# Optimization experiments

Measured on AMD Instinct MI355X. Metric: run time of the kernel, lower is better.

The kernel has to match this reference:

```python
import jax, jax.numpy as jnp
import numpy as np

B, R, C, IC, OC = 32, 16384, 16, 16, 16  # batch, num_routes, num_capsules, in_ch, out_ch
NUM_ITERATIONS = 3


def squash(s, axis=-1):
    # scale * s / norm with scale = norm^2/(1+norm^2)  ==  norm/(1+norm^2) * s
    norm = jnp.linalg.norm(s, axis=axis, keepdims=True)
    return (norm / (1.0 + norm * norm)) * s


def setup_inputs() -> dict:
    key = jax.random.key(0)
    kx, kw = jax.random.split(key)
    x = jax.random.normal(kx, (B, C, IC), dtype=jnp.float32)
    # W param: torch shape (1, R, C, OC, IC); leading 1 squeezed here
    W = jax.random.normal(kw, (R, C, OC, IC), dtype=jnp.float32)
    return {"x": x, "W": W}


def reference(x, W):
    # u_hat[b,r,c,o] = sum_i W[r,c,o,i] * x[b,c,i]   (torch broadcast of x over routes)
    u_hat = jnp.einsum('rcoi,bci->brco', W, x)  # (B, R, C, OC)
    b = jnp.zeros((x.shape[0], R, C, 1), dtype=u_hat.dtype)
    outputs = None
    for it in range(NUM_ITERATIONS):
        c = jax.nn.softmax(b, axis=1)                      # softmax over routes
        s = (c * u_hat).sum(axis=1, keepdims=True)         # (B, 1, C, OC)
        outputs = squash(s)
        if it < NUM_ITERATIONS - 1:
            b = b + (u_hat * outputs).sum(axis=-1, keepdims=True)
    return outputs.squeeze(axis=1)  # (B, C, OC)
```

## Files before the change

### kernel.cpp

```cpp
#include <hip/hip_runtime.h>
#include <math.h>


typedef __attribute__((ext_vector_type(8)))  short short8;
typedef __attribute__((ext_vector_type(16))) float f32x16;

union FU { short8 s; unsigned int u[4]; };

__device__ __forceinline__ void splitpk(float a, float b,
                                        unsigned int& hp, unsigned int& lp) {
    unsigned int ua = __float_as_uint(a), ub = __float_as_uint(b);
    unsigned int ta = ua + 0x7FFFu + ((ua >> 16) & 1u);
    unsigned int tb = ub + 0x7FFFu + ((ub >> 16) & 1u);
    hp = (ta >> 16) | (tb & 0xFFFF0000u);
    float ha = __uint_as_float(ta & 0xFFFF0000u);
    float hb = __uint_as_float(tb & 0xFFFF0000u);
    unsigned int la = __float_as_uint(a - ha) + 0x8000u;
    unsigned int lb = __float_as_uint(b - hb) + 0x8000u;
    lp = (la >> 16) | (lb & 0xFFFF0000u);
}

__global__ __launch_bounds__(256) void k_zero(float* __restrict__ ws) {
    ws[blockIdx.x * 256 + threadIdx.x] = 0.f;
}

__global__ __launch_bounds__(256) void k_wsum(const float4* __restrict__ W4,
                                              float* __restrict__ wsum) {
    int gid = blockIdx.x * 256 + threadIdx.x;
    float4 acc = {0.f, 0.f, 0.f, 0.f};
    int idx = gid;
    #pragma unroll
    for (int it = 0; it < 64; ++it) {
        float4 w = W4[idx];
        acc.x += w.x; acc.y += w.y; acc.z += w.z; acc.w += w.w;
        idx += 262144;
    }
    int cls = gid & 1023;
    atomicAdd(&wsum[cls * 4 + 0], acc.x);
    atomicAdd(&wsum[cls * 4 + 1], acc.y);
    atomicAdd(&wsum[cls * 4 + 2], acc.z);
    atomicAdd(&wsum[cls * 4 + 3], acc.w);
}

__global__ __launch_bounds__(256) void k_v1(const float* __restrict__ wsum,
                                            const float* __restrict__ x,
                                            float* __restrict__ v1) {
    int t = blockIdx.x * 256 + threadIdx.x;
    int o = t & 15, c = (t >> 4) & 15, b = t >> 8;
    const float* xb = x + (b * 16 + c) * 16;
    const float* wr = wsum + (c * 16 + o) * 16;
    float s = 0.f;
    #pragma unroll
    for (int i = 0; i < 16; ++i) s += wr[i] * xb[i];
    s *= (1.0f / 16384.0f);
    float ns = s * s;
    #pragma unroll
    for (int d = 1; d < 16; d <<= 1) ns += __shfl_xor(ns, d);
    v1[t] = s * (sqrtf(ns) / (1.0f + ns));
}

__global__ __launch_bounds__(256) void k_vout_vs(const float* __restrict__ E,
                                                 const float* __restrict__ Z,
                                                 const float* __restrict__ v1,
                                                 float* __restrict__ vs) {
    int t = blockIdx.x * 256 + threadIdx.x;
    float s = E[t] / Z[t >> 4];
    float ns = s * s;
    #pragma unroll
    for (int d = 1; d < 16; d <<= 1) ns += __shfl_xor(ns, d);
    vs[t] = v1[t] + s * (sqrtf(ns) / (1.0f + ns));
}

__global__ __launch_bounds__(256) void k_vout(const float* __restrict__ E,
                                              const float* __restrict__ Z,
                                              float* __restrict__ dst) {
    int t = blockIdx.x * 256 + threadIdx.x;
    float s = E[t] / Z[t >> 4];
    float ns = s * s;
    #pragma unroll
    for (int d = 1; d < 16; d <<= 1) ns += __shfl_xor(ns, d);
    dst[t] = s * (sqrtf(ns) / (1.0f + ns));
}

__global__ __launch_bounds__(512)
void k_iter(const float* __restrict__ W,
            const float* __restrict__ x,
            const float* __restrict__ v,
            float* __restrict__ E,
            float* __restrict__ Z) {
    __shared__ float sV[512];
    __shared__ float E_lds[512];
    __shared__ float Z_lds[32];

    int c = blockIdx.y;
    int r0 = blockIdx.x * 256;
    int tid = threadIdx.x, wv = tid >> 6, l = tid & 63;
    int m  = l & 31;
    int hi = l >> 5;

    { int b = tid >> 4, o = tid & 15;
      sV[tid] = v[b * 256 + c * 16 + o];
      E_lds[tid] = 0.f; }
    if (tid < 32) Z_lds[tid] = 0.f;

    FU bh, bl;
    {
        const float4* xb = (const float4*)x + m * 64 + c * 4 + hi * 2;
        float4 x0 = xb[0], x1 = xb[1];
        splitpk(x0.x, x0.y, bh.u[0], bl.u[0]);
        splitpk(x0.z, x0.w, bh.u[1], bl.u[1]);
        splitpk(x1.x, x1.y, bh.u[2], bl.u[2]);
        splitpk(x1.z, x1.w, bh.u[3], bl.u[3]);
    }
    __syncthreads();

    float vf[16];
    #pragma unroll
    for (int reg = 0; reg < 16; ++reg) {
        int o = (reg & 3) + 4 * hi + 8 * ((reg >> 2) & 1);
        vf[reg] = sV[m * 16 + o];
    }

    float accE[16];
    #pragma unroll
    for (int reg = 0; reg < 16; ++reg) accE[reg] = 0.f;
    float accZ = 0.f;

    const float4* Wb = (const float4*)W +
        ((size_t)(r0 + wv * 2 + (m >> 4)) * 1024 + c * 64 + (m & 15) * 4 + hi * 2);

    float4 ca = Wb[0], cb = Wb[1];

    #pragma unroll
    for (int chunk = 0; chunk < 16; ++chunk) {
        float4 na = ca, nb = cb;
        if (chunk < 15) {
            na = Wb[(size_t)(chunk + 1) * 16384];
            nb = Wb[(size_t)(chunk + 1) * 16384 + 1];
        }

        FU ah, al;
        splitpk(ca.x, ca.y, ah.u[0], al.u[0]);
        splitpk(ca.z, ca.w, ah.u[1], al.u[1]);
        splitpk(cb.x, cb.y, ah.u[2], al.u[2]);
        splitpk(cb.z, cb.w, ah.u[3], al.u[3]);

        f32x16 cf;
        #pragma unroll
        for (int i = 0; i < 16; ++i) cf[i] = 0.f;
        cf = __builtin_amdgcn_mfma_f32_32x32x16_bf16(al.s, bl.s, cf, 0, 0, 0);
        cf = __builtin_amdgcn_mfma_f32_32x32x16_bf16(ah.s, bl.s, cf, 0, 0, 0);
        cf = __builtin_amdgcn_mfma_f32_32x32x16_bf16(al.s, bh.s, cf, 0, 0, 0);
        cf = __builtin_amdgcn_mfma_f32_32x32x16_bf16(ah.s, bh.s, cf, 0, 0, 0);

        float Lp0 = 0.f, Lp1 = 0.f;
        #pragma unroll
        for (int reg = 0; reg < 8; ++reg)  Lp0 += cf[reg] * vf[reg];
        #pragma unroll
        for (int reg = 8; reg < 16; ++reg) Lp1 += cf[reg] * vf[reg];
        float Lv0 = Lp0 + __shfl_xor(Lp0, 32);
        float Lv1 = Lp1 + __shfl_xor(Lp1, 32);
        float e0 = __expf(Lv0), e1 = __expf(Lv1);
        accZ += e0 + e1;
        #pragma unroll
        for (int reg = 0; reg < 8; ++reg)  accE[reg] += e0 * cf[reg];
        #pragma unroll
        for (int reg = 8; reg < 16; ++reg) accE[reg] += e1 * cf[reg];

        ca = na; cb = nb;
    }

    #pragma unroll
    for (int j = 0; j < 8; ++j) {
        int o = (j & 3) + 4 * hi + 8 * (j >> 2);
        atomicAdd(&E_lds[m * 16 + o], accE[j] + accE[j + 8]);
    }
    if (l < 32) atomicAdd(&Z_lds[m], accZ);
    __syncthreads();

    atomicAdd(&E[(tid >> 4) * 256 + c * 16 + (tid & 15)], E_lds[tid]);
    if (tid < 32) atomicAdd(&Z[tid * 16 + c], Z_lds[tid]);
}

extern "C" void kernel_launch(void* const* d_in, const int* in_sizes, int n_in,
                              void* d_out, int out_size, void* d_ws, size_t ws_size,
                              hipStream_t stream) {
    const float* x = (const float*)d_in[0];
    const float* W = (const float*)d_in[1];
    float* out = (float*)d_out;
    float* ws = (float*)d_ws;

    float* wsum = ws + 0;
    float* E2   = ws + 4096;
    float* Z2   = ws + 12288;
    float* E3   = ws + 12800;
    float* Z3   = ws + 20992;
    float* v1   = ws + 21504;
    float* vs   = ws + 29696;

    k_zero<<<84, 256, 0, stream>>>(ws);

    k_wsum<<<1024, 256, 0, stream>>>((const float4*)W, wsum);
    k_v1<<<32, 256, 0, stream>>>(wsum, x, v1);

    k_iter<<<dim3(64, 16), 512, 0, stream>>>(W, x, v1, E2, Z2);
    k_vout_vs<<<32, 256, 0, stream>>>(E2, Z2, v1, vs);

    k_iter<<<dim3(64, 16), 512, 0, stream>>>(W, x, vs, E3, Z3);
    k_vout<<<32, 256, 0, stream>>>(E3, Z3, out);
}
```

Baseline: 214.7 us.

## Stream W tiles through LDS with async global_load_lds four-stage pipeline

Replaces the per-thread register double-buffered W loads in k_iter with direct global-to-LDS async loads (global_load_lds) into a four-slot LDS ring buffer, keeping three chunks in flight. Explicit vmcnt waits gate each chunk before it is read back from LDS. The aim is deeper memory-level parallelism on the W stream, which dominates each iteration kernel. In exchange it adds 64KB of LDS per block, which can lower occupancy, and relies on hand-counted vmcnt values being correct with no block barrier.

```diff
diff --git a/kernel.cpp b/kernel.cpp
--- a/kernel.cpp
+++ b/kernel.cpp
@@ -6,6 +6,9 @@
 typedef __attribute__((ext_vector_type(16))) float f32x16;
 
 union FU { short8 s; unsigned int u[4]; };
+
+typedef const __attribute__((address_space(1))) void GV;
+typedef __attribute__((address_space(3))) void LV;
 
 __device__ __forceinline__ void splitpk(float a, float b,
                                         unsigned int& hp, unsigned int& lp) {
@@ -88,6 +91,7 @@
             const float* __restrict__ v,
             float* __restrict__ E,
             float* __restrict__ Z) {
+    __shared__ float4 Wr[4 * 1024];
     __shared__ float sV[512];
     __shared__ float E_lds[512];
     __shared__ float Z_lds[32];
@@ -126,18 +130,34 @@
     for (int reg = 0; reg < 16; ++reg) accE[reg] = 0.f;
     float accZ = 0.f;
 
-    const float4* Wb = (const float4*)W +
-        ((size_t)(r0 + wv * 2 + (m >> 4)) * 1024 + c * 64 + (m & 15) * 4 + hi * 2);
-
-    float4 ca = Wb[0], cb = Wb[1];
+    asm volatile("s_waitcnt vmcnt(0)" ::: "memory");
+
+    const float4* W4c = (const float4*)W + (size_t)c * 64;
+
+#define STAGE(sl, cn) {                                                        \
+        const float4* s0 = W4c +                                               \
+            (size_t)(r0 + (cn) * 16 + wv * 2 + (m >> 4)) * 1024 +              \
+            (m & 15) * 4 + hi * 2;                                             \
+        __builtin_amdgcn_global_load_lds((GV*)s0,                              \
+            (LV*)&Wr[(sl) * 1024 + wv * 128], 16, 0, 0);                       \
+        __builtin_amdgcn_global_load_lds((GV*)(s0 + 1),                        \
+            (LV*)&Wr[(sl) * 1024 + wv * 128 + 64], 16, 0, 0);                  \
+    }
+
+    STAGE(0, 0); STAGE(1, 1); STAGE(2, 2);
 
     #pragma unroll
     for (int chunk = 0; chunk < 16; ++chunk) {
-        float4 na = ca, nb = cb;
-        if (chunk < 15) {
-            na = Wb[(size_t)(chunk + 1) * 16384];
-            nb = Wb[(size_t)(chunk + 1) * 16384 + 1];
-        }
+        if (chunk <= 12) STAGE((chunk + 3) & 3, chunk + 3);
+
+        if (chunk <= 12)      asm volatile("s_waitcnt vmcnt(6)" ::: "memory");
+        else if (chunk == 13) asm volatile("s_waitcnt vmcnt(4)" ::: "memory");
+        else if (chunk == 14) asm volatile("s_waitcnt vmcnt(2)" ::: "memory");
+        else                  asm volatile("s_waitcnt vmcnt(0)" ::: "memory");
+
+        int sb = (chunk & 3) * 1024 + wv * 128 + l;
+        float4 ca = Wr[sb];
+        float4 cb = Wr[sb + 64];
 
         FU ah, al;
         splitpk(ca.x, ca.y, ah.u[0], al.u[0]);
@@ -166,9 +186,8 @@
         for (int reg = 0; reg < 8; ++reg)  accE[reg] += e0 * cf[reg];
         #pragma unroll
         for (int reg = 8; reg < 16; ++reg) accE[reg] += e1 * cf[reg];
-
-        ca = na; cb = nb;
-    }
+    }
+#undef STAGE
 
     #pragma unroll
     for (int j = 0; j < 8; ++j) {
```

Result: faster. 204.2 us (-4.9%).
